# Optimization experiments

Hardware: AMD Instinct MI355X
Metric: run time of the kernel (lower is better)

## Reference

```python
import jax, jax.numpy as jnp
import numpy as np


def viterbi_decode(emissions, start_trans, trans, end_trans):
    """Batched Viterbi decode (pytorch-crf CRF.decode, full mask).
    emissions: [B,S,T] -> tags [B,S] int32."""
    score0 = start_trans[None, :] + emissions[:, 0]  # [B,T]

    def step(score, em_t):
        nxt = score[:, :, None] + trans[None, :, :]       # [B,T_prev,T_next]
        idx = jnp.argmax(nxt, axis=1)                     # best prev tag per next tag
        best = jnp.max(nxt, axis=1) + em_t                # [B,T]
        return best, idx

    score, hist = jax.lax.scan(step, score0, jnp.swapaxes(emissions[:, 1:], 0, 1))
    last = jnp.argmax(score + end_trans[None, :], axis=1)  # [B]

    def back(tag, h):
        prev = jnp.take_along_axis(h, tag[:, None], axis=1)[:, 0]
        return prev, prev

    _, prevs = jax.lax.scan(back, last, hist, reverse=True)  # [S-1,B]
    return jnp.concatenate([jnp.swapaxes(prevs, 0, 1), last[:, None]], axis=1)


def setup_inputs() -> dict:
    key = jax.random.key(0)
    ks = jax.random.split(key, 10)
    B, S, D, T, L, R = 4, 256, 768, 9, 30, 12
    H = D + L  # 798
    s = lambda d: 1.0 / np.sqrt(d)
    return {
        "embed": jax.random.normal(ks[0], (B, S, D), jnp.float32),
        "linear_w": jax.random.normal(ks[1], (D, T), jnp.float32) * s(D),
        "linear_b": jnp.zeros((T,), jnp.float32),
        "start_trans": jax.random.normal(ks[2], (T,), jnp.float32) * 0.1,
        "trans": jax.random.normal(ks[3], (T, T), jnp.float32) * 0.1,
        "end_trans": jax.random.normal(ks[4], (T,), jnp.float32) * 0.1,
        "label_emb": jax.random.normal(ks[5], (T, L), jnp.float32).at[0].set(0.0),  # padding_idx=0
        "U_w": jax.random.normal(ks[6], (H, H), jnp.float32) * s(H),
        "U_b": jnp.zeros((H,), jnp.float32),
        "W_w": jax.random.normal(ks[7], (H, H), jnp.float32) * s(H),
        "W_b": jnp.zeros((H,), jnp.float32),
        "V_w": jax.random.normal(ks[8], (H, R), jnp.float32) * s(H),
        "none_idx": 0,  # rel2idx['None']
    }


def reference(embed, linear_w, linear_b, start_trans, trans, end_trans,
              label_emb, U_w, U_b, W_w, W_b, V_w, none_idx):
    # NER head (dropout is identity in eval mode)
    ner = embed @ linear_w + linear_b                     # [B,S,T]
    tags = viterbi_decode(ner, start_trans, trans, end_trans)  # [B,S]
    hx = jnp.concatenate([embed, label_emb[tags]], axis=-1)    # [B,S,H]

    # Fused biaffine relation scoring over all (i=target, j=source) pairs:
    # score[b,i,j,:] = V(tanh(U(hx[b,i]) + W(hx[b,j])))
    u = hx @ U_w + U_b                                    # [B,S,H]
    w = hx @ W_w + W_b                                    # [B,S,H]
    pair = jnp.tanh(u[:, :, None, :] + w[:, None, :, :])  # [B,S,S,H]
    scores = jnp.einsum('bijh,hr->bijr', pair, V_w)       # [B,S,S,R]

    # p_head[:, i, rel2idx['None']] = 100 for target i -> diagonal set
    S = embed.shape[1]
    ii = jnp.arange(S)
    scores = scores.at[:, ii, ii, none_idx].set(100.0)
    return tags, scores
```

## Files before the change

kernel.cpp:

```cpp
#include <hip/hip_runtime.h>


typedef unsigned short ushort_t;
typedef __attribute__((ext_vector_type(8))) short bf16x8;
typedef __attribute__((ext_vector_type(4))) float f32x4;
typedef __attribute__((ext_vector_type(2))) float f32x2;
typedef __attribute__((ext_vector_type(4))) int i32x4;
typedef unsigned long long u64;

#define C2F 2.8853900817779268f

#define WS_UW2   0u
#define WS_NER   3276800u
#define WS_VFRAG 3313664u
#define WS_LAB2  3339264u
#define WS_TAGS  3396864u
#define WS_CSUM  3400960u

__device__ __forceinline__ unsigned f2b(float f){
  unsigned u = __float_as_uint(f);
  return (u + 0x7FFFu + ((u>>16)&1u)) >> 16;
}
__device__ __forceinline__ unsigned pkbf16(float hi, float lo){
  return __builtin_amdgcn_perm(__float_as_uint(hi), __float_as_uint(lo), 0x07060302u);
}
__device__ __forceinline__ float lo16(int v){ return __uint_as_float(((unsigned)v)<<16); }
__device__ __forceinline__ float hi16(int v){ return __uint_as_float(((unsigned)v)&0xFFFF0000u); }
__device__ __forceinline__ float hi16g(int v){ return __uint_as_float((unsigned)v); }
__device__ __forceinline__ u64 fcompose(u64 F, u64 H){
  u64 R = 0;
  #pragma unroll
  for (int t=0;t<9;t++){
    unsigned h = (unsigned)(H >> (4*t)) & 15u;
    unsigned v = (unsigned)(F >> (4*h)) & 15u;
    R |= (u64)v << (4*t);
  }
  return R;
}

__global__ __launch_bounds__(256) void gemm_prep_kernel(
    const float* __restrict__ embed, const float* __restrict__ lw,
    const float* __restrict__ lb,    const float* __restrict__ lemb,
    const float* __restrict__ uw,    const float* __restrict__ ub,
    const float* __restrict__ ww,    const float* __restrict__ wb,
    const float* __restrict__ vw,    char* __restrict__ ws)
{
  __shared__ char smem[10496];
  int bx = blockIdx.x, tid = threadIdx.x;
  if (bx < 400) {
    ushort_t (*As)[40] = (ushort_t(*)[40])smem;
    ushort_t (*Bs)[42] = (ushort_t(*)[42])(smem + 5120);
    ushort_t* uw2 = (ushort_t*)(ws + WS_UW2);
    int bm = bx & 15, bn = bx >> 4;
    int M0 = bm*64, N0 = bn*64;
    int w = tid>>6, lane = tid&63;
    int wr = w>>1, wc = w&1;
    int m16 = lane&15, quad = lane>>4;
    int nl = tid>>2, k8 = (tid&3)<<3;
    int bnn = tid & 63, bw = tid >> 6;
    int gn = N0 + bnn;
    const float* bsrc = uw; int bcol = 0; bool bzero = true;
    if (gn < 798)                    { bsrc = uw; bcol = gn;     bzero = false; }
    else if (gn >= 800 && gn < 1598) { bsrc = ww; bcol = gn-800; bzero = false; }

    f32x4 acc[2][2];
    #pragma unroll
    for (int mi=0;mi<2;mi++)
      #pragma unroll
      for (int ni=0;ni<2;ni++) acc[mi][ni] = (f32x4){0.f,0.f,0.f,0.f};

    f32x4 a_lo, a_hi; float bvals[8];
    {
      const float* ap = &embed[(M0+nl)*768 + k8];
      a_lo = *(const f32x4*)ap; a_hi = *(const f32x4*)(ap+4);
      #pragma unroll
      for (int r=0;r<4;r++) {
        int kk = r*8 + bw*2;
        bvals[2*r]   = bzero ? 0.f : bsrc[(kk  )*798 + bcol];
        bvals[2*r+1] = bzero ? 0.f : bsrc[(kk+1)*798 + bcol];
      }
    }
    for (int k0=0; k0<768; k0+=32) {
      i32x4 av = (i32x4){ (int)pkbf16(a_lo.y,a_lo.x), (int)pkbf16(a_lo.w,a_lo.z),
                          (int)pkbf16(a_hi.y,a_hi.x), (int)pkbf16(a_hi.w,a_hi.z) };
      *(i32x4*)&As[nl][k8] = av;
      #pragma unroll
      for (int r=0;r<4;r++) {
        int kk = r*8 + bw*2;
        *(unsigned*)&Bs[bnn][kk] = pkbf16(bvals[2*r+1], bvals[2*r]);
      }
      __syncthreads();
      if (k0 + 32 < 768) {
        const float* ap = &embed[(M0+nl)*768 + k0 + 32 + k8];
        a_lo = *(const f32x4*)ap; a_hi = *(const f32x4*)(ap+4);
        #pragma unroll
        for (int r=0;r<4;r++) {
          int kk = r*8 + bw*2;
          bvals[2*r]   = bzero ? 0.f : bsrc[(k0+32+kk  )*798 + bcol];
          bvals[2*r+1] = bzero ? 0.f : bsrc[(k0+32+kk+1)*798 + bcol];
        }
      }
      bf16x8 a0 = *(const bf16x8*)&As[wr*32      + m16][quad*8];
      bf16x8 a1 = *(const bf16x8*)&As[wr*32 + 16 + m16][quad*8];
      bf16x8 b0 = *(const bf16x8*)&Bs[wc*32      + m16][quad*8];
      bf16x8 b1 = *(const bf16x8*)&Bs[wc*32 + 16 + m16][quad*8];
      acc[0][0] = __builtin_amdgcn_mfma_f32_16x16x32_bf16(a0,b0,acc[0][0],0,0,0);
      acc[0][1] = __builtin_amdgcn_mfma_f32_16x16x32_bf16(a0,b1,acc[0][1],0,0,0);
      acc[1][0] = __builtin_amdgcn_mfma_f32_16x16x32_bf16(a1,b0,acc[1][0],0,0,0);
      acc[1][1] = __builtin_amdgcn_mfma_f32_16x16x32_bf16(a1,b1,acc[1][1],0,0,0);
      __syncthreads();
    }
    #pragma unroll
    for (int mi=0;mi<2;mi++)
      #pragma unroll
      for (int ni=0;ni<2;ni++)
        #pragma unroll
        for (int reg=0;reg<4;reg++) {
          int gm = M0 + wr*32 + mi*16 + quad*4 + reg;
          int go = N0 + wc*32 + ni*16 + m16;
          float bias = 0.f;
          if (go < 798) bias = ub[go];
          else if (go >= 800 && go < 1598) bias = wb[go-800];
          float v = (acc[mi][ni][reg] + bias) * C2F;
          uw2[gm*1600 + go] = (ushort_t)f2b(__builtin_amdgcn_exp2f(v));
        }
  } else if (bx < 450) {
    ushort_t* vf = (ushort_t*)(ws + WS_VFRAG);
    int idx = (bx-400)*256 + tid;
    int jj = idx & 7, lane = (idx>>3) & 63, c = idx >> 9;
    int h = c*32 + ((lane>>4)<<3) + jj;
    int n = lane & 15;
    vf[idx] = (h < 798 && n < 12) ? (ushort_t)f2b(vw[h*12 + n]) : (ushort_t)0;
  } else if (bx < 706) {
    float* ner = (float*)(ws + WS_NER);
    int w = tid >> 6, lane = tid & 63;
    int row = (bx-450)*4 + w;
    float acc[9];
    #pragma unroll
    for (int i=0;i<9;i++) acc[i]=0.f;
    const float* erow = embed + row*768;
    for (int kk=0; kk<12; kk++) {
      int k = kk*64 + lane;
      float e = erow[k];
      #pragma unroll
      for (int i=0;i<9;i++) acc[i] = __builtin_fmaf(e, lw[k*9+i], acc[i]);
    }
    #pragma unroll
    for (int i=0;i<9;i++) {
      float v = acc[i];
      for (int off=32; off>0; off>>=1) v += __shfl_down(v, off);
      if (lane == 0) ner[row*9+i] = v + lb[i];
    }
  } else if (bx < 763) {
    float* lab2 = (float*)(ws + WS_LAB2);
    int idx = (bx-706)*256 + tid;
    if (idx < 14400) {
      int g = idx / 1600, n = idx - g*1600;
      const float* X = (n < 800) ? uw : ww;
      int nn = (n < 800) ? n : (n - 800);
      float v = 1.0f;
      if (nn < 798) {
        float s = 0.f;
        for (int l=0;l<30;l++)
          s = __builtin_fmaf(lemb[g*30+l], X[(768+l)*798 + nn], s);
        v = __builtin_amdgcn_exp2f(s * C2F);
      }
      lab2[idx] = v;
    }
  } else {
    float* csum = (float*)(ws + WS_CSUM);
    if (tid < 12) {
      float s = 0.f;
      for (int h=0;h<798;h++) s += vw[h*12 + tid];
      csum[tid] = s;
    }
  }
}

__global__ __launch_bounds__(256) void viterbi_kernel(
    const float* __restrict__ start_t, const float* __restrict__ trans,
    const float* __restrict__ end_t,
    char* __restrict__ ws, float* __restrict__ out_tags)
{
  __shared__ char smem[46848];
  float* scores = (float*)smem;
  u64* pk = (u64*)(smem + 36864);
  float* trl = (float*)(smem + 45056);
  int* lastArr = (int*)(smem + 45384);
  unsigned char* tagbuf = (unsigned char*)(smem + 45400);
  const float* ner = (const float*)(ws + WS_NER);
  int* tags = (int*)(ws + WS_TAGS);
  int tid = threadIdx.x;
  int w = tid>>6, lane = tid&63;
  int b = w;
  int tt = lane < 9 ? lane : 8;
  if (tid < 81) trl[tid] = trans[tid];

  float tcol[9];
  #pragma unroll
  for (int p=0;p<9;p++) tcol[p] = trans[p*9+tt];
  const float* nb = ner + (b*256)*9 + tt;
  float score = start_t[tt] + nb[0];
  if (lane < 9) scores[(b*256 + 0)*9 + tt] = score;

  float cur[15], nxt[15];
  #pragma unroll
  for (int j=0;j<15;j++) cur[j] = nb[(1+j)*9];
  #define RL(p) (__uint_as_float(__builtin_amdgcn_readlane(__float_as_uint(score), p)) + tcol[p])
  for (int ch=0; ch<17; ch++) {
    int sb = 1 + ch*15;
    if (ch < 16) {
      #pragma unroll
      for (int j=0;j<15;j++) nxt[j] = nb[(sb+15+j)*9];
    }
    #pragma unroll
    for (int j=0;j<15;j++) {
      float m0 = fmaxf(fmaxf(RL(0),RL(1)),RL(2));
      float m1 = fmaxf(fmaxf(RL(3),RL(4)),RL(5));
      float m2 = fmaxf(fmaxf(RL(6),RL(7)),RL(8));
      score = fmaxf(fmaxf(m0,m1),m2) + cur[j];
      if (lane < 9) scores[(b*256 + sb + j)*9 + tt] = score;
    }
    #pragma unroll
    for (int j=0;j<15;j++) cur[j] = nxt[j];
  }
  {
    float fin = score + end_t[tt];
    #define RLF(p) __uint_as_float(__builtin_amdgcn_readlane(__float_as_uint(fin), p))
    float bv = RLF(0); int ba = 0;
    #pragma unroll
    for (int p=1;p<9;p++) { float v = RLF(p); if (v > bv) { bv = v; ba = p; } }
    if (lane == 0) lastArr[b] = ba;
    #undef RLF
  }
  #undef RL
  __syncthreads();

  for (int idx = tid; idx < 1024; idx += 256) {
    int bb = idx >> 8, s = idx & 255;
    u64 f;
    if (s == 255) f = 0x876543210ULL;
    else {
      const float* srow = &scores[(bb*256 + s)*9];
      float sp[9];
      #pragma unroll
      for (int p=0;p<9;p++) sp[p] = srow[p];
      f = 0;
      #pragma unroll
      for (int t=0;t<9;t++) {
        float best = sp[0] + trl[t]; int arg = 0;
        #pragma unroll
        for (int p=1;p<9;p++) {
          float v = sp[p] + trl[p*9 + t];
          if (v > best) { best = v; arg = p; }
        }
        f |= (u64)arg << (4*t);
      }
    }
    pk[bb*256 + s] = f;
  }
  __syncthreads();

  if (tid < 64) {
    int cb = tid >> 4, c = tid & 15;
    u64 fs[16];
    #pragma unroll
    for (int j=0;j<16;j++) fs[j] = pk[cb*256 + c*16 + j];
    u64 G = fs[15];
    #pragma unroll
    for (int j=14;j>=0;j--) G = fcompose(fs[j], G);
    u64 F = G;
    #pragma unroll
    for (int d=1; d<16; d<<=1) {
      u64 H = __shfl(F, tid + d);
      if (c + d < 16) F = fcompose(F, H);
    }
    int last = lastArr[cb];
    u64 Hn = __shfl(F, (c==15) ? tid : tid+1);
    unsigned t_cur = (c==15) ? (unsigned)last
                             : (unsigned)((Hn >> (4*last)) & 15u);
    #pragma unroll
    for (int j=15;j>=0;j--) {
      t_cur = (unsigned)((fs[j] >> (4*t_cur)) & 15u);
      tagbuf[cb*256 + c*16 + j] = (unsigned char)t_cur;
    }
  }
  __syncthreads();

  for (int idx = tid; idx < 1024; idx += 256) {
    int tg = (int)tagbuf[idx];
    tags[idx] = tg;
    out_tags[idx] = (float)tg;
  }
}

__device__ __forceinline__ unsigned rpair(int uvw, int wvw){
  f32x2 xu; xu.x = lo16(uvw); xu.y = hi16g(uvw);
  f32x2 xw; xw.x = lo16(wvw); xw.y = hi16g(wvw);
  f32x2 one2 = {1.0f, 1.0f};
  f32x2 p;
  asm("v_pk_fma_f32 %0, %1, %2, %3" : "=v"(p) : "v"(xu), "v"(xw), "v"(one2));
  unsigned pb = __builtin_amdgcn_perm(__float_as_uint(p.y), __float_as_uint(p.x), 0x07060302u);
  unsigned magic2 = 0x7EF37EF3u;
  unsigned y;
  asm("v_pk_sub_u16 %0, %1, %2" : "=v"(y) : "v"(magic2), "v"(pb));
  return y;
}

__global__ __launch_bounds__(512) void scorer_kernel(
    char* __restrict__ ws, const int* __restrict__ none_p,
    float* __restrict__ d_out)
{
  __shared__ ushort_t su[16][804];
  __shared__ ushort_t sw[16][804];
  const ushort_t* uw2 = (const ushort_t*)(ws + WS_UW2);
  const float* lab2   = (const float*)(ws + WS_LAB2);
  const ushort_t* vf  = (const ushort_t*)(ws + WS_VFRAG);
  const int* tags     = (const int*)(ws + WS_TAGS);
  const float* csum   = (const float*)(ws + WS_CSUM);
  float* out_sc = d_out + 1024;
  int bx = blockIdx.x, tid = threadIdx.x;
  int b = bx >> 8, ti = (bx>>4)&15, tj = bx&15;
  int I0 = ti*16, J0 = tj*16, bS = b*256;

  for (int idx = tid; idx < 1600; idx += 512) {
    int row = idx / 100, c8 = idx - row*100, kc = c8*8;
    int grow = bS + I0 + row;
    int tag = tags[grow];
    i32x4 uv = *(const i32x4*)(uw2 + (size_t)grow*1600 + kc);
    const float* lp = lab2 + tag*1600 + kc;
    f32x4 l0 = *(const f32x4*)lp;
    f32x4 l1 = *(const f32x4*)(lp+4);
    i32x4 q = (i32x4){ (int)pkbf16(hi16g(uv.x)*l0.y, lo16(uv.x)*l0.x),
                       (int)pkbf16(hi16g(uv.y)*l0.w, lo16(uv.y)*l0.z),
                       (int)pkbf16(hi16g(uv.z)*l1.y, lo16(uv.z)*l1.x),
                       (int)pkbf16(hi16g(uv.w)*l1.w, lo16(uv.w)*l1.z) };
    *(i32x4*)&su[row][kc] = q;
  }
  for (int idx = tid; idx < 1600; idx += 512) {
    int row = idx / 100, c8 = idx - row*100, kc = c8*8;
    int grow = bS + J0 + row;
    int tag = tags[grow];
    i32x4 uv = *(const i32x4*)(uw2 + (size_t)grow*1600 + 800 + kc);
    const float* lp = lab2 + tag*1600 + 800 + kc;
    f32x4 l0 = *(const f32x4*)lp;
    f32x4 l1 = *(const f32x4*)(lp+4);
    i32x4 q = (i32x4){ (int)pkbf16(hi16g(uv.x)*l0.y, lo16(uv.x)*l0.x),
                       (int)pkbf16(hi16g(uv.y)*l0.w, lo16(uv.y)*l0.z),
                       (int)pkbf16(hi16g(uv.z)*l1.y, lo16(uv.z)*l1.x),
                       (int)pkbf16(hi16g(uv.w)*l1.w, lo16(uv.w)*l1.z) };
    *(i32x4*)&sw[row][kc] = q;
  }
  __syncthreads();

  int lane = tid & 63, w = tid >> 6;
  int m16 = lane & 15, quad = lane >> 4;
  int none = *none_p;

  f32x4 acc[2];
  acc[0] = (f32x4){0.f,0.f,0.f,0.f};
  acc[1] = (f32x4){0.f,0.f,0.f,0.f};

  const ushort_t* vlane = vf + lane*8;
  i32x4 bfc = *(const i32x4*)vlane;
  for (int c=0; c<25; c++) {
    i32x4 bfn;
    if (c < 24) bfn = *(const i32x4*)(vlane + (c+1)*512);
    int koff = c*32 + quad*8;
    i32x4 wv = *(const i32x4*)&sw[m16][koff];
    bf16x8 bfrag = __builtin_bit_cast(bf16x8, bfc);
    #pragma unroll
    for (int it=0; it<2; it++) {
      i32x4 uv = *(const i32x4*)&su[w*2+it][koff];
      unsigned a0 = rpair(uv.x, wv.x);
      unsigned a1 = rpair(uv.y, wv.y);
      unsigned a2 = rpair(uv.z, wv.z);
      unsigned a3 = rpair(uv.w, wv.w);
      i32x4 avv = (i32x4){(int)a0,(int)a1,(int)a2,(int)a3};
      bf16x8 af = __builtin_bit_cast(bf16x8, avv);
      acc[it] = __builtin_amdgcn_mfma_f32_16x16x32_bf16(af, bfrag, acc[it], 0,0,0);
    }
    bfc = bfn;
  }

  int r = m16;
  if (r < 12) {
    float cs = csum[r];
    #pragma unroll
    for (int it=0; it<2; it++) {
      int gi = I0 + w*2 + it;
      #pragma unroll
      for (int reg=0; reg<4; reg++) {
        int gj = J0 + quad*4 + reg;
        float v = __builtin_fmaf(-2.0f, acc[it][reg], cs);
        if (gi == gj && r == none) v = 100.0f;
        out_sc[(size_t)((bS + gi)*256 + gj)*12 + r] = v;
      }
    }
  }
}

extern "C" void kernel_launch(void* const* d_in, const int* in_sizes, int n_in,
                              void* d_out, int out_size, void* d_ws, size_t ws_size,
                              hipStream_t stream)
{
  const float* embed = (const float*)d_in[0];
  const float* lw    = (const float*)d_in[1];
  const float* lb    = (const float*)d_in[2];
  const float* st    = (const float*)d_in[3];
  const float* tr    = (const float*)d_in[4];
  const float* et    = (const float*)d_in[5];
  const float* lemb  = (const float*)d_in[6];
  const float* uw    = (const float*)d_in[7];
  const float* ub    = (const float*)d_in[8];
  const float* ww    = (const float*)d_in[9];
  const float* wb    = (const float*)d_in[10];
  const float* vw    = (const float*)d_in[11];
  const int* none_p  = (const int*)d_in[12];
  char* ws = (char*)d_ws;
  float* out = (float*)d_out;

  hipLaunchKernelGGL(gemm_prep_kernel, dim3(764), dim3(256), 0, stream,
                     embed, lw, lb, lemb, uw, ub, ww, wb, vw, ws);
  hipLaunchKernelGGL(viterbi_kernel, dim3(1), dim3(256), 0, stream,
                     st, tr, et, ws, out);
  hipLaunchKernelGGL(scorer_kernel, dim3(1024), dim3(512), 0, stream,
                     ws, none_p, out);
}
```

Measured before the change: 167.1 us.

## Precompute label-scaled U/W rows in a separate kernel; read U rows from global

Adds a fuse_kernel that applies the per-tag label scaling to the bf16 U/W projection rows once, in place, after Viterbi. Before this, every scorer block redid that scaling for its own rows. The scorer now copies only the W tile into LDS and reads the U rows straight from global memory inside the MFMA loop, which halves shared memory use and may allow more blocks per CU. The cost is an extra kernel launch and a full read-modify-write pass over the workspace, plus global loads on the inner loop's critical path.

```diff
diff --git a/kernel.cpp b/kernel.cpp
--- a/kernel.cpp
+++ b/kernel.cpp
@@ -25,7 +25,6 @@
   return __builtin_amdgcn_perm(__float_as_uint(hi), __float_as_uint(lo), 0x07060302u);
 }
 __device__ __forceinline__ float lo16(int v){ return __uint_as_float(((unsigned)v)<<16); }
-__device__ __forceinline__ float hi16(int v){ return __uint_as_float(((unsigned)v)&0xFFFF0000u); }
 __device__ __forceinline__ float hi16g(int v){ return __uint_as_float((unsigned)v); }
 __device__ __forceinline__ u64 fcompose(u64 F, u64 H){
   u64 R = 0;
@@ -294,6 +293,26 @@
   }
 }
 
+__global__ __launch_bounds__(256) void fuse_kernel(char* __restrict__ ws)
+{
+  ushort_t* uw2      = (ushort_t*)(ws + WS_UW2);
+  const float* lab2  = (const float*)(ws + WS_LAB2);
+  const int* tags    = (const int*)(ws + WS_TAGS);
+  int idx = blockIdx.x*256 + threadIdx.x;
+  int row = idx / 200, c8 = idx - row*200, kc = c8*8;
+  int tag = tags[row];
+  ushort_t* p = uw2 + (size_t)row*1600 + kc;
+  i32x4 uv = *(const i32x4*)p;
+  const float* lp = lab2 + tag*1600 + kc;
+  f32x4 l0 = *(const f32x4*)lp;
+  f32x4 l1 = *(const f32x4*)(lp+4);
+  i32x4 q = (i32x4){ (int)pkbf16(hi16g(uv.x)*l0.y, lo16(uv.x)*l0.x),
+                     (int)pkbf16(hi16g(uv.y)*l0.w, lo16(uv.y)*l0.z),
+                     (int)pkbf16(hi16g(uv.z)*l1.y, lo16(uv.z)*l1.x),
+                     (int)pkbf16(hi16g(uv.w)*l1.w, lo16(uv.w)*l1.z) };
+  *(i32x4*)p = q;
+}
+
 __device__ __forceinline__ unsigned rpair(int uvw, int wvw){
   f32x2 xu; xu.x = lo16(uvw); xu.y = hi16g(uvw);
   f32x2 xw; xw.x = lo16(wvw); xw.y = hi16g(wvw);
@@ -311,12 +330,9 @@
     char* __restrict__ ws, const int* __restrict__ none_p,
     float* __restrict__ d_out)
 {
-  __shared__ ushort_t su[16][804];
   __shared__ ushort_t sw[16][804];
   const ushort_t* uw2 = (const ushort_t*)(ws + WS_UW2);
-  const float* lab2   = (const float*)(ws + WS_LAB2);
   const ushort_t* vf  = (const ushort_t*)(ws + WS_VFRAG);
-  const int* tags     = (const int*)(ws + WS_TAGS);
   const float* csum   = (const float*)(ws + WS_CSUM);
   float* out_sc = d_out + 1024;
   int bx = blockIdx.x, tid = threadIdx.x;
@@ -325,31 +341,8 @@
 
   for (int idx = tid; idx < 1600; idx += 512) {
     int row = idx / 100, c8 = idx - row*100, kc = c8*8;
-    int grow = bS + I0 + row;
-    int tag = tags[grow];
-    i32x4 uv = *(const i32x4*)(uw2 + (size_t)grow*1600 + kc);
-    const float* lp = lab2 + tag*1600 + kc;
-    f32x4 l0 = *(const f32x4*)lp;
-    f32x4 l1 = *(const f32x4*)(lp+4);
-    i32x4 q = (i32x4){ (int)pkbf16(hi16g(uv.x)*l0.y, lo16(uv.x)*l0.x),
-                       (int)pkbf16(hi16g(uv.y)*l0.w, lo16(uv.y)*l0.z),
-                       (int)pkbf16(hi16g(uv.z)*l1.y, lo16(uv.z)*l1.x),
-                       (int)pkbf16(hi16g(uv.w)*l1.w, lo16(uv.w)*l1.z) };
-    *(i32x4*)&su[row][kc] = q;
-  }
-  for (int idx = tid; idx < 1600; idx += 512) {
-    int row = idx / 100, c8 = idx - row*100, kc = c8*8;
     int grow = bS + J0 + row;
-    int tag = tags[grow];
-    i32x4 uv = *(const i32x4*)(uw2 + (size_t)grow*1600 + 800 + kc);
-    const float* lp = lab2 + tag*1600 + 800 + kc;
-    f32x4 l0 = *(const f32x4*)lp;
-    f32x4 l1 = *(const f32x4*)(lp+4);
-    i32x4 q = (i32x4){ (int)pkbf16(hi16g(uv.x)*l0.y, lo16(uv.x)*l0.x),
-                       (int)pkbf16(hi16g(uv.y)*l0.w, lo16(uv.y)*l0.z),
-                       (int)pkbf16(hi16g(uv.z)*l1.y, lo16(uv.z)*l1.x),
-                       (int)pkbf16(hi16g(uv.w)*l1.w, lo16(uv.w)*l1.z) };
-    *(i32x4*)&sw[row][kc] = q;
+    *(i32x4*)&sw[row][kc] = *(const i32x4*)(uw2 + (size_t)grow*1600 + 800 + kc);
   }
   __syncthreads();
 
@@ -361,6 +354,8 @@
   acc[0] = (f32x4){0.f,0.f,0.f,0.f};
   acc[1] = (f32x4){0.f,0.f,0.f,0.f};
 
+  const ushort_t* su0 = uw2 + (size_t)(bS + I0 + w*2    )*1600 + quad*8;
+  const ushort_t* su1 = uw2 + (size_t)(bS + I0 + w*2 + 1)*1600 + quad*8;
   const ushort_t* vlane = vf + lane*8;
   i32x4 bfc = *(const i32x4*)vlane;
   for (int c=0; c<25; c++) {
@@ -368,17 +363,26 @@
     if (c < 24) bfn = *(const i32x4*)(vlane + (c+1)*512);
     int koff = c*32 + quad*8;
     i32x4 wv = *(const i32x4*)&sw[m16][koff];
+    i32x4 uv0 = *(const i32x4*)(su0 + c*32);
+    i32x4 uv1 = *(const i32x4*)(su1 + c*32);
     bf16x8 bfrag = __builtin_bit_cast(bf16x8, bfc);
-    #pragma unroll
-    for (int it=0; it<2; it++) {
-      i32x4 uv = *(const i32x4*)&su[w*2+it][koff];
-      unsigned a0 = rpair(uv.x, wv.x);
-      unsigned a1 = rpair(uv.y, wv.y);
-      unsigned a2 = rpair(uv.z, wv.z);
-      unsigned a3 = rpair(uv.w, wv.w);
+    {
+      unsigned a0 = rpair(uv0.x, wv.x);
+      unsigned a1 = rpair(uv0.y, wv.y);
+      unsigned a2 = rpair(uv0.z, wv.z);
+      unsigned a3 = rpair(uv0.w, wv.w);
       i32x4 avv = (i32x4){(int)a0,(int)a1,(int)a2,(int)a3};
       bf16x8 af = __builtin_bit_cast(bf16x8, avv);
-      acc[it] = __builtin_amdgcn_mfma_f32_16x16x32_bf16(af, bfrag, acc[it], 0,0,0);
+      acc[0] = __builtin_amdgcn_mfma_f32_16x16x32_bf16(af, bfrag, acc[0], 0,0,0);
+    }
+    {
+      unsigned a0 = rpair(uv1.x, wv.x);
+      unsigned a1 = rpair(uv1.y, wv.y);
+      unsigned a2 = rpair(uv1.z, wv.z);
+      unsigned a3 = rpair(uv1.w, wv.w);
+      i32x4 avv = (i32x4){(int)a0,(int)a1,(int)a2,(int)a3};
+      bf16x8 af = __builtin_bit_cast(bf16x8, avv);
+      acc[1] = __builtin_amdgcn_mfma_f32_16x16x32_bf16(af, bfrag, acc[1], 0,0,0);
     }
     bfc = bfn;
   }
@@ -424,6 +428,7 @@
                      embed, lw, lb, lemb, uw, ub, ww, wb, vw, ws);
   hipLaunchKernelGGL(viterbi_kernel, dim3(1), dim3(256), 0, stream,
                      st, tr, et, ws, out);
+  hipLaunchKernelGGL(fuse_kernel, dim3(800), dim3(256), 0, stream, ws);
   hipLaunchKernelGGL(scorer_kernel, dim3(1024), dim3(512), 0, stream,
                      ws, none_p, out);
 }
```

After: 167.0 us. Within noise of the previous version (-0.1%).
